# Kernel optimization log

Hardware: AMD Instinct MI355X
Metric: run time of the kernel (lower is better)

## Reference

```python
import jax, jax.numpy as jnp
import numpy as np

B, K, Z = 16384, 4096, 64  # batch, codebook size, code dim


def _linear_params(key, fan_in, fan_out):
    kw, kb = jax.random.split(key)
    lim = 1.0 / np.sqrt(fan_in)
    W = jax.random.uniform(kw, (fan_out, fan_in), jnp.float32, -lim, lim)
    b = jax.random.uniform(kb, (fan_out,), jnp.float32, -lim, lim)
    return W, b


def setup_inputs() -> dict:
    key = jax.random.key(0)
    ks = jax.random.split(key, 10)
    X = jax.random.normal(ks[0], (B, 784), jnp.float32)
    We1, be1 = _linear_params(ks[1], 784, 1000)
    We2, be2 = _linear_params(ks[2], 1000, 500)
    We3, be3 = _linear_params(ks[3], 500, 300)
    We4, be4 = _linear_params(ks[4], 300, Z)
    emb = jax.random.normal(ks[5], (K, Z), jnp.float32)  # nn.Embedding default N(0,1)
    Wd1, bd1 = _linear_params(ks[6], Z, 300)
    Wd2, bd2 = _linear_params(ks[7], 300, 500)
    Wd3, bd3 = _linear_params(ks[8], 500, 1000)
    Wd4, bd4 = _linear_params(ks[9], 1000, 784)
    return dict(X=X, We1=We1, be1=be1, We2=We2, be2=be2, We3=We3, be3=be3,
                We4=We4, be4=be4, emb=emb, Wd1=Wd1, bd1=bd1, Wd2=Wd2, bd2=bd2,
                Wd3=Wd3, bd3=bd3, Wd4=Wd4, bd4=bd4)


def _lin(x, W, b):
    return x @ W.T + b


def _nearest(query, target):
    # squared euclidean distances [Q, T] via expanded form (same math, no QxTxZ blowup)
    q2 = jnp.sum(query * query, axis=1, keepdims=True)        # [Q,1]
    t2 = jnp.sum(target * target, axis=1)                      # [T]
    d = q2 - 2.0 * (query @ target.T) + t2[None, :]            # [Q,T]
    idx = jnp.argmin(d, axis=1)                                # first min, like torch .min
    return target[idx]


def reference(X, We1, be1, We2, be2, We3, be3, We4, be4, emb,
              Wd1, bd1, Wd2, bd2, Wd3, bd3, Wd4, bd4):
    x = X.reshape(-1, 784)
    h = jax.nn.relu(_lin(x, We1, be1))
    h = jax.nn.relu(_lin(h, We2, be2))
    h = jax.nn.relu(_lin(h, We3, be3))
    Z_enc = _lin(h, We4, be4)                                  # [B,Z]
    Z_emb = _nearest(Z_enc, emb)                               # [B,Z]
    d = jax.nn.leaky_relu(_lin(Z_emb, Wd1, bd1), 0.1)
    d = jax.nn.leaky_relu(_lin(d, Wd2, bd2), 0.1)
    d = jax.nn.leaky_relu(_lin(d, Wd3, bd3), 0.1)
    Z_dec = jnp.tanh(_lin(d, Wd4, bd4)).reshape(-1, 1, 28, 28)
    Z_enc_for_emb = _nearest(emb, Z_enc)                       # [K,Z]
    return (Z_dec, Z_enc, Z_dec, Z_enc_for_emb)
```

## Files before the change

### kernel.cpp

```cpp
#include <hip/hip_runtime.h>
#include <hip/hip_bf16.h>
#include <math.h>

typedef __bf16 bf16_t;
typedef __bf16 bf16x8 __attribute__((ext_vector_type(8)));
typedef __bf16 bf16x4 __attribute__((ext_vector_type(4)));
typedef float f32x4 __attribute__((ext_vector_type(4)));

template<int ACT, int RB>
__global__ __launch_bounds__(256)
void np_gemm(const float* __restrict__ A, const float* __restrict__ W,
             const float* __restrict__ bias, float* __restrict__ C,
             int N, int K)
{
    __shared__ __align__(16) float sA[16][RB * 64];
    __shared__ __align__(16) float sB[16][128];
    const int tid  = threadIdx.x;
    const int tx   = tid & 15, ty = tid >> 4;
    const int bRow = blockIdx.y * (RB * 64), bCol = blockIdx.x * 128;

    float4 acc[RB][2][4];
#pragma unroll
    for (int ib = 0; ib < RB; ++ib)
#pragma unroll
        for (int jb = 0; jb < 2; ++jb)
#pragma unroll
            for (int i = 0; i < 4; ++i)
                acc[ib][jb][i] = make_float4(0.f, 0.f, 0.f, 0.f);

    for (int k0 = 0; k0 < K; k0 += 16) {
        __syncthreads();
#pragma unroll
        for (int i = 0; i < RB; ++i) {
            int c  = tid + i * 256;
            int r  = c >> 2;
            int kc = (c & 3) << 2;
            int gk = k0 + kc;
            float4 av = make_float4(0.f, 0.f, 0.f, 0.f);
            if (gk < K) av = *(const float4*)(A + (size_t)(bRow + r) * K + gk);
            sA[kc + 0][r] = av.x; sA[kc + 1][r] = av.y;
            sA[kc + 2][r] = av.z; sA[kc + 3][r] = av.w;
        }
#pragma unroll
        for (int i = 0; i < 2; ++i) {
            int c  = tid + i * 256;
            int r  = c >> 2;
            int kc = (c & 3) << 2;
            int gk = k0 + kc;
            int gr = bCol + r;
            float4 bv = make_float4(0.f, 0.f, 0.f, 0.f);
            if (gr < N && gk < K) bv = *(const float4*)(W + (size_t)gr * K + gk);
            sB[kc + 0][r] = bv.x; sB[kc + 1][r] = bv.y;
            sB[kc + 2][r] = bv.z; sB[kc + 3][r] = bv.w;
        }
        __syncthreads();

#pragma unroll
        for (int kk = 0; kk < 16; ++kk) {
            float4 a[RB], b[2];
#pragma unroll
            for (int ib = 0; ib < RB; ++ib)
                a[ib] = *(const float4*)&sA[kk][ib * 64 + ty * 4];
            b[0] = *(const float4*)&sB[kk][tx * 4];
            b[1] = *(const float4*)&sB[kk][64 + tx * 4];
#pragma unroll
            for (int ib = 0; ib < RB; ++ib) {
                float ai[4] = {a[ib].x, a[ib].y, a[ib].z, a[ib].w};
#pragma unroll
                for (int i = 0; i < 4; ++i)
#pragma unroll
                    for (int jb = 0; jb < 2; ++jb) {
                        acc[ib][jb][i].x = __fmaf_rn(ai[i], b[jb].x, acc[ib][jb][i].x);
                        acc[ib][jb][i].y = __fmaf_rn(ai[i], b[jb].y, acc[ib][jb][i].y);
                        acc[ib][jb][i].z = __fmaf_rn(ai[i], b[jb].z, acc[ib][jb][i].z);
                        acc[ib][jb][i].w = __fmaf_rn(ai[i], b[jb].w, acc[ib][jb][i].w);
                    }
            }
        }
    }

#pragma unroll
    for (int jb = 0; jb < 2; ++jb) {
        int col = bCol + jb * 64 + tx * 4;
        if (col >= N) continue;
        float4 bb = *(const float4*)(bias + col);
#pragma unroll
        for (int ib = 0; ib < RB; ++ib)
#pragma unroll
            for (int i = 0; i < 4; ++i) {
                int row = bRow + ib * 64 + ty * 4 + i;
                float4 v = acc[ib][jb][i];
                float4 o;
                o.x = __fadd_rn(v.x, bb.x); o.y = __fadd_rn(v.y, bb.y);
                o.z = __fadd_rn(v.z, bb.z); o.w = __fadd_rn(v.w, bb.w);
                if (ACT == 1) {
                    o.x = o.x > 0.f ? o.x : 0.f; o.y = o.y > 0.f ? o.y : 0.f;
                    o.z = o.z > 0.f ? o.z : 0.f; o.w = o.w > 0.f ? o.w : 0.f;
                }
                *(float4*)(C + (size_t)row * N + col) = o;
            }
    }
}

#define BM 128
#define BN 128
#define BKK 32
template<int ACT, int TERMS>
__global__ __launch_bounds__(256)
void gemm_bt(const float* __restrict__ A, const float* __restrict__ W,
             const float* __restrict__ bias,
             float* __restrict__ C0, float* __restrict__ C1,
             int N, int K)
{
    __shared__ __align__(16) bf16_t sA[TERMS][BM][BKK];
    __shared__ __align__(16) bf16_t sB[TERMS][BN][BKK];

    const int tid  = threadIdx.x;
    const int bRow = blockIdx.y * BM;
    const int bCol = blockIdx.x * BN;
    const int wave = tid >> 6;
    const int lane = tid & 63;
    const int wr   = (wave >> 1) * 64;
    const int wc   = (wave & 1) * 64;
    const int quad = lane >> 4;
    const int l15  = lane & 15;

    f32x4 acc[4][4];
#pragma unroll
    for (int i = 0; i < 4; ++i)
#pragma unroll
        for (int j = 0; j < 4; ++j) acc[i][j] = (f32x4){0.f, 0.f, 0.f, 0.f};

    for (int k0 = 0; k0 < K; k0 += BKK) {
        __syncthreads();
#pragma unroll
        for (int i = 0; i < 4; ++i) {
            int c   = tid + i * 256;
            int r   = c >> 3;
            int col = (c & 7) << 2;
            int gk  = k0 + col;
            float4 v = make_float4(0.f, 0.f, 0.f, 0.f);
            if (gk < K) v = *(const float4*)(A + (size_t)(bRow + r) * K + gk);
            float e[4] = {v.x, v.y, v.z, v.w};
#pragma unroll
            for (int t = 0; t < TERMS; ++t) {
                bf16x4 hv;
#pragma unroll
                for (int u = 0; u < 4; ++u) {
                    hv[u] = (bf16_t)e[u];
                    e[u] -= (float)hv[u];
                }
                *(bf16x4*)&sA[t][r][col] = hv;
            }
        }
#pragma unroll
        for (int i = 0; i < 4; ++i) {
            int c   = tid + i * 256;
            int r   = c >> 3;
            int col = (c & 7) << 2;
            int gk  = k0 + col;
            int gr  = bCol + r;
            float4 v = make_float4(0.f, 0.f, 0.f, 0.f);
            if (gr < N && gk < K) v = *(const float4*)(W + (size_t)gr * K + gk);
            float e[4] = {v.x, v.y, v.z, v.w};
#pragma unroll
            for (int t = 0; t < TERMS; ++t) {
                bf16x4 hv;
#pragma unroll
                for (int u = 0; u < 4; ++u) {
                    hv[u] = (bf16_t)e[u];
                    e[u] -= (float)hv[u];
                }
                *(bf16x4*)&sB[t][r][col] = hv;
            }
        }
        __syncthreads();

        bf16x8 af[TERMS][4], bfr[TERMS][4];
#pragma unroll
        for (int t = 0; t < TERMS; ++t)
#pragma unroll
            for (int i = 0; i < 4; ++i) {
                af[t][i]  = *(const bf16x8*)&sA[t][wr + i * 16 + l15][quad * 8];
                bfr[t][i] = *(const bf16x8*)&sB[t][wc + i * 16 + l15][quad * 8];
            }
#pragma unroll
        for (int i = 0; i < 4; ++i)
#pragma unroll
            for (int j = 0; j < 4; ++j)
#pragma unroll
                for (int ta = 0; ta < TERMS; ++ta)
#pragma unroll
                    for (int tb = 0; tb < TERMS - ta; ++tb)
                        acc[i][j] = __builtin_amdgcn_mfma_f32_16x16x32_bf16(
                            af[ta][i], bfr[tb][j], acc[i][j], 0, 0, 0);
    }

#pragma unroll
    for (int j = 0; j < 4; ++j) {
        int col = bCol + wc + j * 16 + l15;
        if (col >= N) continue;
        float bv = bias[col];
#pragma unroll
        for (int i = 0; i < 4; ++i) {
#pragma unroll
            for (int r = 0; r < 4; ++r) {
                int row = bRow + wr + i * 16 + quad * 4 + r;
                float v = acc[i][j][r] + bv;
                if (ACT == 1)      v = v > 0.f ? v : 0.f;
                else if (ACT == 2) v = v >= 0.f ? v : 0.1f * v;
                else if (ACT == 3) v = tanhf(v);
                size_t o = (size_t)row * N + col;
                C0[o] = v;
                if (C1) C1[o] = v;
            }
        }
    }
}

__global__ __launch_bounds__(256)
void k_nearest(const float* __restrict__ Q, const float* __restrict__ C,
               const float* __restrict__ q2a, const float* __restrict__ cn2,
               int chunk, float* __restrict__ pd, int* __restrict__ pi)
{
    __shared__ __align__(16) float sc[64][64];
    __shared__ __align__(16) float sn[64];
    const int tid = threadIdx.x;
    const int q   = blockIdx.x * 256 + tid;
    const int G   = gridDim.y;

    float qr[64];
    const float4* qp = (const float4*)(Q + (size_t)q * 64);
#pragma unroll
    for (int i = 0; i < 16; ++i) ((float4*)qr)[i] = qp[i];
    const float q2 = q2a[q];

    float best = 3.4e38f;
    int   bi   = 0x7fffffff;
    const int c0 = blockIdx.y * chunk;

    for (int cb = 0; cb < chunk; cb += 64) {
        __syncthreads();
        const float4* gp = (const float4*)(C + (size_t)(c0 + cb) * 64);
#pragma unroll
        for (int i = 0; i < 4; ++i) {
            int e = tid + i * 256;
            ((float4*)&sc[0][0])[e] = gp[e];
        }
        if (tid < 64) sn[tid] = cn2[c0 + cb + tid];
        __syncthreads();

        for (int c = 0; c < 64; c += 4) {
            float a0 = 0.f, a1 = 0.f, a2 = 0.f, a3 = 0.f;
            const float4* e0 = (const float4*)&sc[c + 0][0];
            const float4* e1 = (const float4*)&sc[c + 1][0];
            const float4* e2p = (const float4*)&sc[c + 2][0];
            const float4* e3 = (const float4*)&sc[c + 3][0];
#pragma unroll
            for (int z = 0; z < 16; ++z) {
                float4 q4 = ((float4*)qr)[z];
                float4 v0 = e0[z], v1 = e1[z], v2 = e2p[z], v3 = e3[z];
                a0 = __fmaf_rn(q4.x, v0.x, a0); a0 = __fmaf_rn(q4.y, v0.y, a0);
                a0 = __fmaf_rn(q4.z, v0.z, a0); a0 = __fmaf_rn(q4.w, v0.w, a0);
                a1 = __fmaf_rn(q4.x, v1.x, a1); a1 = __fmaf_rn(q4.y, v1.y, a1);
                a1 = __fmaf_rn(q4.z, v1.z, a1); a1 = __fmaf_rn(q4.w, v1.w, a1);
                a2 = __fmaf_rn(q4.x, v2.x, a2); a2 = __fmaf_rn(q4.y, v2.y, a2);
                a2 = __fmaf_rn(q4.z, v2.z, a2); a2 = __fmaf_rn(q4.w, v2.w, a2);
                a3 = __fmaf_rn(q4.x, v3.x, a3); a3 = __fmaf_rn(q4.y, v3.y, a3);
                a3 = __fmaf_rn(q4.z, v3.z, a3); a3 = __fmaf_rn(q4.w, v3.w, a3);
            }
            float d;
            d = __fadd_rn(__fsub_rn(q2, __fmul_rn(2.f, a0)), sn[c + 0]);
            if (d < best) { best = d; bi = c0 + cb + c + 0; }
            d = __fadd_rn(__fsub_rn(q2, __fmul_rn(2.f, a1)), sn[c + 1]);
            if (d < best) { best = d; bi = c0 + cb + c + 1; }
            d = __fadd_rn(__fsub_rn(q2, __fmul_rn(2.f, a2)), sn[c + 2]);
            if (d < best) { best = d; bi = c0 + cb + c + 2; }
            d = __fadd_rn(__fsub_rn(q2, __fmul_rn(2.f, a3)), sn[c + 3]);
            if (d < best) { best = d; bi = c0 + cb + c + 3; }
        }
    }
    pd[(size_t)q * G + blockIdx.y] = best;
    pi[(size_t)q * G + blockIdx.y] = bi;
}

__global__ void k_reduce(const float* __restrict__ pd, const int* __restrict__ pi,
                         int G, int NQ, int* __restrict__ out)
{
    int q = blockIdx.x * blockDim.x + threadIdx.x;
    if (q >= NQ) return;
    float best = 3.4e38f; int bi = 0;
    for (int g = 0; g < G; ++g) {
        float d = pd[(size_t)q * G + g];
        if (d < best) { best = d; bi = pi[(size_t)q * G + g]; }
    }
    out[q] = bi;
}

__global__ void k_gather(const float* __restrict__ src, const int* __restrict__ idx,
                         float* __restrict__ dst, int nsrc)
{
    int r = blockIdx.x, z = threadIdx.x;
    int i = idx[r];
    i = i < 0 ? 0 : (i >= nsrc ? nsrc - 1 : i);
    dst[(size_t)r * 64 + z] = src[(size_t)i * 64 + z];
}

__global__ void k_norm2(const float* __restrict__ s, float* __restrict__ o, int rows)
{
    int r0 = blockIdx.x * blockDim.x + threadIdx.x;
    if (r0 >= rows) return;
    const float* p = s + (size_t)r0 * 64;
    float r[8];
#pragma unroll
    for (int j = 0; j < 8; ++j) r[j] = __fmul_rn(p[j], p[j]);
#pragma unroll
    for (int i = 8; i < 64; i += 8)
#pragma unroll
        for (int j = 0; j < 8; ++j)
            r[j] = __fadd_rn(r[j], __fmul_rn(p[i + j], p[i + j]));
    float t01 = __fadd_rn(r[0], r[1]), t23 = __fadd_rn(r[2], r[3]);
    float t45 = __fadd_rn(r[4], r[5]), t67 = __fadd_rn(r[6], r[7]);
    o[r0] = __fadd_rn(__fadd_rn(t01, t23), __fadd_rn(t45, t67));
}

extern "C" void kernel_launch(void* const* d_in, const int* in_sizes, int n_in,
                              void* d_out, int out_size, void* d_ws, size_t ws_size,
                              hipStream_t stream)
{
    const int B  = 16384;
    const int KC = 4096;

    const float* X   = (const float*)d_in[0];
    const float* We1 = (const float*)d_in[1];
    const float* be1 = (const float*)d_in[2];
    const float* We2 = (const float*)d_in[3];
    const float* be2 = (const float*)d_in[4];
    const float* We3 = (const float*)d_in[5];
    const float* be3 = (const float*)d_in[6];
    const float* We4 = (const float*)d_in[7];
    const float* be4 = (const float*)d_in[8];
    const float* emb = (const float*)d_in[9];
    const float* Wd1 = (const float*)d_in[10];
    const float* bd1 = (const float*)d_in[11];
    const float* Wd2 = (const float*)d_in[12];
    const float* bd2 = (const float*)d_in[13];
    const float* Wd3 = (const float*)d_in[14];
    const float* bd3 = (const float*)d_in[15];
    const float* Wd4 = (const float*)d_in[16];
    const float* bd4 = (const float*)d_in[17];

    float* out = (float*)d_out;
    const size_t OFF1 = (size_t)B * 784;
    const size_t OFF2 = OFF1 + (size_t)B * 64;
    const size_t OFF3 = OFF2 + (size_t)B * 784;
    float* zenc = out + OFF1;

    const size_t FIXED = (size_t)12 << 20;
    int MQ;
    if      (ws_size >= FIXED + (size_t)16384 * 7200) MQ = 16384;
    else if (ws_size >= FIXED + (size_t)8192  * 7200) MQ = 8192;
    else                                              MQ = 4096;
    const int NQn = B / MQ;

    char* ws = (char*)d_ws;
    size_t off = 0;
    auto alloc = [&](size_t bytes) -> void* {
        void* p = ws + off;
        off = (off + bytes + 255) & ~(size_t)255;
        return p;
    };
    float* pd    = (float*)alloc((size_t)262144 * 4);
    int*   pi    = (int*)alloc((size_t)262144 * 4);
    int*   idx1  = (int*)alloc((size_t)B * 4);
    int*   idx2  = (int*)alloc((size_t)KC * 4);
    float* e2    = (float*)alloc((size_t)KC * 4);
    float* z2    = (float*)alloc((size_t)B * 4);
    float* zemb  = (float*)alloc((size_t)B * 64 * 4);
    float* h1    = (float*)alloc((size_t)MQ * 1000 * 4);
    float* h2    = (float*)alloc((size_t)MQ * 500 * 4);
    float* h3    = (float*)alloc((size_t)MQ * 300 * 4);
    float* d1f   = h3;
    float* d2f   = h2;
    float* d3f   = h1;

    dim3 blk(256);
    const dim3 eg1(8, MQ / 128), eg2(4, MQ / 64), eg3(3, MQ / 64), eg4(1, MQ / 64);
    const dim3 dq1(3, MQ / 128), dq2(4, MQ / 128), dq3(8, MQ / 128), dq4(7, MQ / 128);

    for (int q = 0; q < NQn; ++q) {
        const float* Xq = X + (size_t)q * MQ * 784;
        np_gemm<1, 2><<<eg1, blk, 0, stream>>>(Xq, We1, be1, h1, 1000, 784);
        np_gemm<1, 1><<<eg2, blk, 0, stream>>>(h1, We2, be2, h2, 500, 1000);
        np_gemm<1, 1><<<eg3, blk, 0, stream>>>(h2, We3, be3, h3, 300, 500);
        np_gemm<0, 1><<<eg4, blk, 0, stream>>>(h3, We4, be4,
                                               zenc + (size_t)q * MQ * 64, 64, 300);
    }

    k_norm2<<<dim3((KC + 255) / 256), blk, 0, stream>>>(emb, e2, KC);
    k_norm2<<<dim3((B + 255) / 256),  blk, 0, stream>>>(zenc, z2, B);

    k_nearest<<<dim3(64, 16), blk, 0, stream>>>(zenc, emb, z2, e2, 256, pd, pi);
    k_reduce <<<dim3(B / 256), blk, 0, stream>>>(pd, pi, 16, B, idx1);
    k_gather <<<dim3(B), dim3(64), 0, stream>>>(emb, idx1, zemb, KC);

    k_nearest<<<dim3(16, 64), blk, 0, stream>>>(emb, zenc, e2, z2, 256, pd, pi);
    k_reduce <<<dim3(KC / 256), blk, 0, stream>>>(pd, pi, 64, KC, idx2);
    k_gather <<<dim3(KC), dim3(64), 0, stream>>>(zenc, idx2, out + OFF3, B);

    for (int q = 0; q < NQn; ++q) {
        const float* zq = zemb + (size_t)q * MQ * 64;
        gemm_bt<2, 2><<<dq1, blk, 0, stream>>>(zq,  Wd1, bd1, d1f, nullptr, 300,  64);
        gemm_bt<2, 2><<<dq2, blk, 0, stream>>>(d1f, Wd2, bd2, d2f, nullptr, 500,  300);
        gemm_bt<2, 2><<<dq3, blk, 0, stream>>>(d2f, Wd3, bd3, d3f, nullptr, 1000, 500);
        gemm_bt<3, 2><<<dq4, blk, 0, stream>>>(d3f, Wd4, bd4,
                                               out + (size_t)q * MQ * 784,
                                               out + OFF2 + (size_t)q * MQ * 784, 784, 1000);
    }

    (void)in_sizes; (void)n_in; (void)out_size;
}
```

Before: 1.656 ms.

## Pre-split decoder operands into bf16 hi/lo planes and load via direct-to-LDS

The decoder GEMMs now read precomputed bf16 hi/lo planes, padded to tile-friendly widths, for weights and activations. Each GEMM epilogue writes its output already split into planes for the next layer, and tiles are loaded with global_load_lds 16-byte transfers instead of fp32 loads plus in-kernel conversion. The fp32 encoder GEMM also gets padded shared-memory strides to avoid bank conflicts. This removes repeated per-tile split work and register staging, at the cost of extra weight-split kernels per call, padded compute, and bf16 intermediate storage.

```diff
diff --git a/kernel.cpp b/kernel.cpp
--- a/kernel.cpp
+++ b/kernel.cpp
@@ -6,6 +6,13 @@
 typedef __bf16 bf16x8 __attribute__((ext_vector_type(8)));
 typedef __bf16 bf16x4 __attribute__((ext_vector_type(4)));
 typedef float f32x4 __attribute__((ext_vector_type(4)));
+
+__device__ __forceinline__ void gload16(const void* g, void* l)
+{
+    __builtin_amdgcn_global_load_lds(
+        (const __attribute__((address_space(1))) void*)g,
+        (__attribute__((address_space(3))) void*)l, 16, 0, 0);
+}
 
 template<int ACT, int RB>
 __global__ __launch_bounds__(256)
@@ -13,8 +20,10 @@
              const float* __restrict__ bias, float* __restrict__ C,
              int N, int K)
 {
-    __shared__ __align__(16) float sA[16][RB * 64];
-    __shared__ __align__(16) float sB[16][128];
+    constexpr int LDA = RB * 64 + 4;
+    constexpr int LDB = 128 + 4;
+    __shared__ __align__(16) float sA[16][LDA];
+    __shared__ __align__(16) float sB[16][LDB];
     const int tid  = threadIdx.x;
     const int tx   = tid & 15, ty = tid >> 4;
     const int bRow = blockIdx.y * (RB * 64), bCol = blockIdx.x * 128;
@@ -102,22 +111,33 @@
     }
 }
 
-#define BM 128
-#define BN 128
-#define BKK 32
-template<int ACT, int TERMS>
+__global__ void k_split(const float* __restrict__ src, bf16_t* __restrict__ hi,
+                        bf16_t* __restrict__ lo, int rows, int K, int rowsP, int Kp)
+{
+    int e = blockIdx.x * 256 + threadIdx.x;
+    if (e >= rowsP * Kp) return;
+    int r = e / Kp, k = e - r * Kp;
+    float v = (r < rows && k < K) ? src[(size_t)r * K + k] : 0.f;
+    bf16_t h = (bf16_t)v;
+    bf16_t l = (bf16_t)(v - (float)h);
+    hi[e] = h; lo[e] = l;
+}
+
+template<int ACT, int OUT>
 __global__ __launch_bounds__(256)
-void gemm_bt(const float* __restrict__ A, const float* __restrict__ W,
-             const float* __restrict__ bias,
-             float* __restrict__ C0, float* __restrict__ C1,
-             int N, int K)
-{
-    __shared__ __align__(16) bf16_t sA[TERMS][BM][BKK];
-    __shared__ __align__(16) bf16_t sB[TERMS][BN][BKK];
+void gemm_planes(const bf16_t* __restrict__ Ahi, const bf16_t* __restrict__ Alo,
+                 const bf16_t* __restrict__ Bhi, const bf16_t* __restrict__ Blo,
+                 const float* __restrict__ bias,
+                 float* __restrict__ C0, float* __restrict__ C1,
+                 bf16_t* __restrict__ Phi, bf16_t* __restrict__ Plo,
+                 int N, int Kp, int Kpn)
+{
+    __shared__ __align__(16) bf16_t sA[2][128][32];
+    __shared__ __align__(16) bf16_t sB[2][128][32];
 
     const int tid  = threadIdx.x;
-    const int bRow = blockIdx.y * BM;
-    const int bCol = blockIdx.x * BN;
+    const int bRow = blockIdx.y * 128;
+    const int bCol = blockIdx.x * 128;
     const int wave = tid >> 6;
     const int lane = tid & 63;
     const int wr   = (wave >> 1) * 64;
@@ -131,54 +151,25 @@
 #pragma unroll
         for (int j = 0; j < 4; ++j) acc[i][j] = (f32x4){0.f, 0.f, 0.f, 0.f};
 
-    for (int k0 = 0; k0 < K; k0 += BKK) {
-        __syncthreads();
-#pragma unroll
-        for (int i = 0; i < 4; ++i) {
-            int c   = tid + i * 256;
-            int r   = c >> 3;
-            int col = (c & 7) << 2;
-            int gk  = k0 + col;
-            float4 v = make_float4(0.f, 0.f, 0.f, 0.f);
-            if (gk < K) v = *(const float4*)(A + (size_t)(bRow + r) * K + gk);
-            float e[4] = {v.x, v.y, v.z, v.w};
-#pragma unroll
-            for (int t = 0; t < TERMS; ++t) {
-                bf16x4 hv;
-#pragma unroll
-                for (int u = 0; u < 4; ++u) {
-                    hv[u] = (bf16_t)e[u];
-                    e[u] -= (float)hv[u];
-                }
-                *(bf16x4*)&sA[t][r][col] = hv;
-            }
-        }
-#pragma unroll
-        for (int i = 0; i < 4; ++i) {
-            int c   = tid + i * 256;
-            int r   = c >> 3;
-            int col = (c & 7) << 2;
-            int gk  = k0 + col;
-            int gr  = bCol + r;
-            float4 v = make_float4(0.f, 0.f, 0.f, 0.f);
-            if (gr < N && gk < K) v = *(const float4*)(W + (size_t)gr * K + gk);
-            float e[4] = {v.x, v.y, v.z, v.w};
-#pragma unroll
-            for (int t = 0; t < TERMS; ++t) {
-                bf16x4 hv;
-#pragma unroll
-                for (int u = 0; u < 4; ++u) {
-                    hv[u] = (bf16_t)e[u];
-                    e[u] -= (float)hv[u];
-                }
-                *(bf16x4*)&sB[t][r][col] = hv;
-            }
-        }
-        __syncthreads();
-
-        bf16x8 af[TERMS][4], bfr[TERMS][4];
-#pragma unroll
-        for (int t = 0; t < TERMS; ++t)
+    for (int k0 = 0; k0 < Kp; k0 += 32) {
+        __syncthreads();
+#pragma unroll
+        for (int i = 0; i < 2; ++i) {
+            int c    = tid + i * 256;
+            int row  = c >> 2;
+            int koff = (c & 3) << 3;
+            size_t ga = (size_t)(bRow + row) * Kp + (k0 + koff);
+            size_t gb = (size_t)(bCol + row) * Kp + (k0 + koff);
+            gload16(Ahi + ga, &sA[0][row][koff]);
+            gload16(Alo + ga, &sA[1][row][koff]);
+            gload16(Bhi + gb, &sB[0][row][koff]);
+            gload16(Blo + gb, &sB[1][row][koff]);
+        }
+        __syncthreads();
+
+        bf16x8 af[2][4], bfr[2][4];
+#pragma unroll
+        for (int t = 0; t < 2; ++t)
 #pragma unroll
             for (int i = 0; i < 4; ++i) {
                 af[t][i]  = *(const bf16x8*)&sA[t][wr + i * 16 + l15][quad * 8];
@@ -189,9 +180,9 @@
 #pragma unroll
             for (int j = 0; j < 4; ++j)
 #pragma unroll
-                for (int ta = 0; ta < TERMS; ++ta)
-#pragma unroll
-                    for (int tb = 0; tb < TERMS - ta; ++tb)
+                for (int ta = 0; ta < 2; ++ta)
+#pragma unroll
+                    for (int tb = 0; tb < 2 - ta; ++tb)
                         acc[i][j] = __builtin_amdgcn_mfma_f32_16x16x32_bf16(
                             af[ta][i], bfr[tb][j], acc[i][j], 0, 0, 0);
     }
@@ -199,21 +190,43 @@
 #pragma unroll
     for (int j = 0; j < 4; ++j) {
         int col = bCol + wc + j * 16 + l15;
-        if (col >= N) continue;
-        float bv = bias[col];
-#pragma unroll
-        for (int i = 0; i < 4; ++i) {
-#pragma unroll
-            for (int r = 0; r < 4; ++r) {
-                int row = bRow + wr + i * 16 + quad * 4 + r;
-                float v = acc[i][j][r] + bv;
-                if (ACT == 1)      v = v > 0.f ? v : 0.f;
-                else if (ACT == 2) v = v >= 0.f ? v : 0.1f * v;
-                else if (ACT == 3) v = tanhf(v);
-                size_t o = (size_t)row * N + col;
-                C0[o] = v;
-                if (C1) C1[o] = v;
-            }
+        if (OUT == 0) {
+            if (col >= N) continue;
+            float bv = bias[col];
+#pragma unroll
+            for (int i = 0; i < 4; ++i)
+#pragma unroll
+                for (int r = 0; r < 4; ++r) {
+                    int row = bRow + wr + i * 16 + quad * 4 + r;
+                    float v = acc[i][j][r] + bv;
+                    if (ACT == 1)      v = v > 0.f ? v : 0.f;
+                    else if (ACT == 2) v = v >= 0.f ? v : 0.1f * v;
+                    else if (ACT == 3) v = tanhf(v);
+                    size_t o = (size_t)row * N + col;
+                    C0[o] = v;
+                    if (C1) C1[o] = v;
+                }
+        } else {
+            if (col >= Kpn) continue;
+            const bool real = col < N;
+            float bv = real ? bias[col] : 0.f;
+#pragma unroll
+            for (int i = 0; i < 4; ++i)
+#pragma unroll
+                for (int r = 0; r < 4; ++r) {
+                    int row = bRow + wr + i * 16 + quad * 4 + r;
+                    float v = 0.f;
+                    if (real) {
+                        v = acc[i][j][r] + bv;
+                        if (ACT == 1)      v = v > 0.f ? v : 0.f;
+                        else if (ACT == 2) v = v >= 0.f ? v : 0.1f * v;
+                        else if (ACT == 3) v = tanhf(v);
+                    }
+                    bf16_t h = (bf16_t)v;
+                    bf16_t l = (bf16_t)(v - (float)h);
+                    size_t o = (size_t)row * Kpn + col;
+                    Phi[o] = h; Plo[o] = l;
+                }
         }
     }
 }
@@ -306,6 +319,19 @@
     dst[(size_t)r * 64 + z] = src[(size_t)i * 64 + z];
 }
 
+__global__ void k_gather_split(const float* __restrict__ src, const int* __restrict__ idx,
+                               bf16_t* __restrict__ hi, bf16_t* __restrict__ lo, int nsrc)
+{
+    int r = blockIdx.x, z = threadIdx.x;
+    int i = idx[r];
+    i = i < 0 ? 0 : (i >= nsrc ? nsrc - 1 : i);
+    float v = src[(size_t)i * 64 + z];
+    bf16_t h = (bf16_t)v;
+    bf16_t l = (bf16_t)(v - (float)h);
+    hi[(size_t)r * 64 + z] = h;
+    lo[(size_t)r * 64 + z] = l;
+}
+
 __global__ void k_norm2(const float* __restrict__ s, float* __restrict__ o, int rows)
 {
     int r0 = blockIdx.x * blockDim.x + threadIdx.x;
@@ -356,10 +382,10 @@
     const size_t OFF3 = OFF2 + (size_t)B * 784;
     float* zenc = out + OFF1;
 
-    const size_t FIXED = (size_t)12 << 20;
+    const size_t FIXED = (size_t)16 << 20;
     int MQ;
-    if      (ws_size >= FIXED + (size_t)16384 * 7200) MQ = 16384;
-    else if (ws_size >= FIXED + (size_t)8192  * 7200) MQ = 8192;
+    if      (ws_size >= FIXED + (size_t)16384 * 7424) MQ = 16384;
+    else if (ws_size >= FIXED + (size_t)8192  * 7424) MQ = 8192;
     else                                              MQ = 4096;
     const int NQn = B / MQ;
 
@@ -376,17 +402,35 @@
     int*   idx2  = (int*)alloc((size_t)KC * 4);
     float* e2    = (float*)alloc((size_t)KC * 4);
     float* z2    = (float*)alloc((size_t)B * 4);
-    float* zemb  = (float*)alloc((size_t)B * 64 * 4);
-    float* h1    = (float*)alloc((size_t)MQ * 1000 * 4);
-    float* h2    = (float*)alloc((size_t)MQ * 500 * 4);
-    float* h3    = (float*)alloc((size_t)MQ * 300 * 4);
-    float* d1f   = h3;
-    float* d2f   = h2;
-    float* d3f   = h1;
+    bf16_t* zembh = (bf16_t*)alloc((size_t)B * 64 * 2);
+    bf16_t* zembl = (bf16_t*)alloc((size_t)B * 64 * 2);
+    bf16_t* wp1h = (bf16_t*)alloc((size_t)384 * 64 * 2);
+    bf16_t* wp1l = (bf16_t*)alloc((size_t)384 * 64 * 2);
+    bf16_t* wp2h = (bf16_t*)alloc((size_t)512 * 320 * 2);
+    bf16_t* wp2l = (bf16_t*)alloc((size_t)512 * 320 * 2);
+    bf16_t* wp3h = (bf16_t*)alloc((size_t)1024 * 512 * 2);
+    bf16_t* wp3l = (bf16_t*)alloc((size_t)1024 * 512 * 2);
+    bf16_t* wp4h = (bf16_t*)alloc((size_t)896 * 1024 * 2);
+    bf16_t* wp4l = (bf16_t*)alloc((size_t)896 * 1024 * 2);
+    char* big = (char*)alloc((size_t)MQ * 7424);
+    float* h1 = (float*)big;
+    float* h2 = (float*)(big + (size_t)MQ * 4000);
+    float* h3 = (float*)(big + (size_t)MQ * 6000);
+    bf16_t* d1h = (bf16_t*)big;
+    bf16_t* d1l = (bf16_t*)(big + (size_t)MQ * 640);
+    bf16_t* d2h = (bf16_t*)(big + (size_t)MQ * 1280);
+    bf16_t* d2l = (bf16_t*)(big + (size_t)MQ * 2304);
+    bf16_t* d3h = (bf16_t*)(big + (size_t)MQ * 3328);
+    bf16_t* d3l = (bf16_t*)(big + (size_t)MQ * 5376);
 
     dim3 blk(256);
     const dim3 eg1(8, MQ / 128), eg2(4, MQ / 64), eg3(3, MQ / 64), eg4(1, MQ / 64);
     const dim3 dq1(3, MQ / 128), dq2(4, MQ / 128), dq3(8, MQ / 128), dq4(7, MQ / 128);
+
+    k_split<<<dim3((384 * 64    + 255) / 256), blk, 0, stream>>>(Wd1, wp1h, wp1l, 300, 64, 384, 64);
+    k_split<<<dim3((512 * 320   + 255) / 256), blk, 0, stream>>>(Wd2, wp2h, wp2l, 500, 300, 512, 320);
+    k_split<<<dim3((1024 * 512  + 255) / 256), blk, 0, stream>>>(Wd3, wp3h, wp3l, 1000, 500, 1024, 512);
+    k_split<<<dim3((896 * 1024  + 255) / 256), blk, 0, stream>>>(Wd4, wp4h, wp4l, 784, 1000, 896, 1024);
 
     for (int q = 0; q < NQn; ++q) {
         const float* Xq = X + (size_t)q * MQ * 784;
@@ -402,20 +446,24 @@
 
     k_nearest<<<dim3(64, 16), blk, 0, stream>>>(zenc, emb, z2, e2, 256, pd, pi);
     k_reduce <<<dim3(B / 256), blk, 0, stream>>>(pd, pi, 16, B, idx1);
-    k_gather <<<dim3(B), dim3(64), 0, stream>>>(emb, idx1, zemb, KC);
+    k_gather_split<<<dim3(B), dim3(64), 0, stream>>>(emb, idx1, zembh, zembl, KC);
 
     k_nearest<<<dim3(16, 64), blk, 0, stream>>>(emb, zenc, e2, z2, 256, pd, pi);
     k_reduce <<<dim3(KC / 256), blk, 0, stream>>>(pd, pi, 64, KC, idx2);
     k_gather <<<dim3(KC), dim3(64), 0, stream>>>(zenc, idx2, out + OFF3, B);
 
     for (int q = 0; q < NQn; ++q) {
-        const float* zq = zemb + (size_t)q * MQ * 64;
-        gemm_bt<2, 2><<<dq1, blk, 0, stream>>>(zq,  Wd1, bd1, d1f, nullptr, 300,  64);
-        gemm_bt<2, 2><<<dq2, blk, 0, stream>>>(d1f, Wd2, bd2, d2f, nullptr, 500,  300);
-        gemm_bt<2, 2><<<dq3, blk, 0, stream>>>(d2f, Wd3, bd3, d3f, nullptr, 1000, 500);
-        gemm_bt<3, 2><<<dq4, blk, 0, stream>>>(d3f, Wd4, bd4,
-                                               out + (size_t)q * MQ * 784,
-                                               out + OFF2 + (size_t)q * MQ * 784, 784, 1000);
+        gemm_planes<2, 1><<<dq1, blk, 0, stream>>>(
+            zembh + (size_t)q * MQ * 64, zembl + (size_t)q * MQ * 64,
+            wp1h, wp1l, bd1, nullptr, nullptr, d1h, d1l, 300, 64, 320);
+        gemm_planes<2, 1><<<dq2, blk, 0, stream>>>(
+            d1h, d1l, wp2h, wp2l, bd2, nullptr, nullptr, d2h, d2l, 500, 320, 512);
+        gemm_planes<2, 1><<<dq3, blk, 0, stream>>>(
+            d2h, d2l, wp3h, wp3l, bd3, nullptr, nullptr, d3h, d3l, 1000, 512, 1024);
+        gemm_planes<3, 0><<<dq4, blk, 0, stream>>>(
+            d3h, d3l, wp4h, wp4l, bd4,
+            out + (size_t)q * MQ * 784, out + OFF2 + (size_t)q * MQ * 784,
+            nullptr, nullptr, 784, 1024, 0);
     }
 
     (void)in_sizes; (void)n_in; (void)out_size;
```

New measurement: 1.424 ms. 1.16x faster.
